# Kernel optimization log

Hardware: AMD Instinct MI355X
Metric: run time of the kernel (lower is better)

Reference implementation:

```python
import jax, jax.numpy as jnp
import numpy as np

B, S, D, H, DK = 32, 1024, 256, 8, 32
MASK_VALUE = -1e-30  # note: NOT -inf; masked scores become ~0 pre-softmax, faithful to source


def setup_inputs() -> dict:
    key = jax.random.key(0)
    ks = jax.random.split(key, 7)
    query = jax.random.normal(ks[0], (B, S, D), dtype=jnp.float32)
    key_t = jax.random.normal(ks[1], (B, S, D), dtype=jnp.float32)
    value = jax.random.normal(ks[2], (B, S, D), dtype=jnp.float32)
    # binary observation mask over key positions
    mask = (jax.random.uniform(ks[3], (B, S)) > 0.5).astype(jnp.float32)
    glorot = jax.nn.initializers.glorot_uniform(in_axis=1, out_axis=2)
    Wq = glorot(ks[4], (H, D, DK), jnp.float32)
    Wk = glorot(ks[5], (H, D, DK), jnp.float32)
    Wv = glorot(ks[6], (H, D, DK), jnp.float32)
    return {"query": query, "key": key_t, "value": value, "mask": mask,
            "Wq": Wq, "Wk": Wk, "Wv": Wv}


def reference(query, key, value, mask, Wq, Wk, Wv):
    # per-head projections, vectorized over heads: [B,S,D] x [H,D,DK] -> [B,H,S,DK]
    q = jnp.einsum('bsd,hdk->bhsk', query, Wq)
    k = jnp.einsum('bsd,hdk->bhsk', key, Wk)
    v = jnp.einsum('bsd,hdk->bhsk', value, Wv)
    # raw scores (no 1/sqrt(dk) scaling in source): [B,H,Sq,Sk]
    A = jnp.einsum('bhqk,bhsk->bhqs', q, k)
    m = mask[:, None, None, :]  # [B,1,1,Sk]
    A = m * A + (1.0 - m) * MASK_VALUE  # multiplicative mask, NOT additive
    A = jax.nn.softmax(A, axis=-1)
    out = jnp.einsum('bhqs,bhsk->bhqk', A, v)  # [B,H,Sq,DK]
    # concat heads along last dim, matching torch.cat order
    return out.transpose(0, 2, 1, 3).reshape(B, S, H * DK)
```

## Files before the change

### kernel.cpp

```cpp
#include <hip/hip_runtime.h>
#include <math.h>

#define B_  32
#define S_  1024
#define D_  256
#define H_  8
#define DK_ 32
#define MASKV (-1e-30f)
#define LOG2E 1.44269504f

typedef __attribute__((ext_vector_type(4))) short bf4_t;
typedef __attribute__((ext_vector_type(8))) short bf8_t;
typedef __attribute__((ext_vector_type(4))) float f4_t;

__device__ __forceinline__ unsigned fbits(float x) {
    union { float f; unsigned u; } v; v.f = x; return v.u;
}
__device__ __forceinline__ float bitsf(unsigned u) {
    union { unsigned u; float f; } v; v.u = u; return v.f;
}

#if __has_builtin(__builtin_amdgcn_exp2f)
#define EXP2F(x) __builtin_amdgcn_exp2f(x)
#else
#define EXP2F(x) __expf((x) * 0.69314718f)
#endif

__device__ __forceinline__ void gld16(const void* g, void* l) {
    __builtin_amdgcn_global_load_lds(
        (const __attribute__((address_space(1))) void*)g,
        (__attribute__((address_space(3))) void*)l, 16, 0, 0);
}

#define PSEL 0x07060302u


__global__ __launch_bounds__(256) void prep_w(
    const float* __restrict__ Wq, const float* __restrict__ Wk,
    const float* __restrict__ Wv, short* __restrict__ WpH, short* __restrict__ WpL)
{
    const int a = blockIdx.x >> 3;
    const int h = blockIdx.x & 7;
    const float* W = (a == 0 ? Wq : (a == 1 ? Wk : Wv)) + (size_t)h * 256 * 32;
    const int t = threadIdx.x;
    const int k    = t & 31;
    const int dgrp = t >> 5;
    const int ng   = h * 2 + (k >> 4);
    const int l15  = k & 15;
#pragma unroll
    for (int jj = blockIdx.y * 2; jj < blockIdx.y * 2 + 2; ++jj) {
        const int d0 = jj * 32 + dgrp * 4;
        float x[4];
#pragma unroll
        for (int r = 0; r < 4; ++r) x[r] = W[(size_t)(d0 + r) * 32 + k];
        unsigned hu[4], lu[4];
#pragma unroll
        for (int r = 0; r < 4; ++r) {
            unsigned hb = (fbits(x[r]) + 0x8000u) & 0xFFFF0000u;
            hu[r] = hb;
            lu[r] = fbits(x[r] - bitsf(hb)) + 0x8000u;
        }
        uint2 hp = make_uint2(__builtin_amdgcn_perm(hu[1], hu[0], PSEL),
                              __builtin_amdgcn_perm(hu[3], hu[2], PSEL));
        uint2 lp = make_uint2(__builtin_amdgcn_perm(lu[1], lu[0], PSEL),
                              __builtin_amdgcn_perm(lu[3], lu[2], PSEL));
        const int quad = (d0 >> 3) & 3;
        const int jb   = d0 & 7;
        size_t off = (size_t)a * 65536
                   + ((size_t)(jj * 16 + ng) * 64 + quad * 16 + l15) * 8 + jb;
        *(uint2*)&WpH[off] = hp;
        *(uint2*)&WpL[off] = lp;
    }
}

__global__ __launch_bounds__(256) void proj_kernel(
    const float* __restrict__ Xq, const float* __restrict__ Xk,
    const float* __restrict__ Xv, const float* __restrict__ mask,
    const short* __restrict__ WpH, const short* __restrict__ WpL,
    short* __restrict__ qpH, short* __restrict__ qpL,
    short* __restrict__ kpH, short* __restrict__ kpL,
    short* __restrict__ vpT)
{
    __shared__ __align__(16) short XsH[8192];
    __shared__ __align__(16) short XsL[8192];

    const int a  = blockIdx.y;
    const float* X = (a == 0 ? Xq : (a == 1 ? Xk : Xv));
    const short* WH = WpH + (size_t)a * 65536;
    const short* WL = WpL + (size_t)a * 65536;
    const int m0 = blockIdx.x * 64;

    const int tid  = threadIdx.x;
    const int lane = tid & 63;
    const int wv   = tid >> 6;
    const int l15  = lane & 15;
    const int quad = lane >> 4;

    f4_t acc[4][4];
#pragma unroll
    for (int i = 0; i < 4; ++i)
#pragma unroll
        for (int j = 0; j < 4; ++j) acc[i][j] = (f4_t){0.f, 0.f, 0.f, 0.f};

    const int r    = tid >> 2;
    const int dseg = tid & 3;
    const int tix  = r >> 4;
    const int rl15 = r & 15;

    for (int h2 = 0; h2 < 2; ++h2) {
        __syncthreads();
        {
            const float* xp = X + (size_t)(m0 + r) * 256 + h2 * 128 + dseg * 32;
#pragma unroll
            for (int q = 0; q < 4; ++q) {
                float4 x0 = *(const float4*)(xp + q * 8);
                float4 x1 = *(const float4*)(xp + q * 8 + 4);
                float xv[8] = {x0.x, x0.y, x0.z, x0.w, x1.x, x1.y, x1.z, x1.w};
                bf8_t hi, lo;
#pragma unroll
                for (int j = 0; j < 8; ++j) {
                    unsigned hu = (fbits(xv[j]) + 0x8000u) & 0xFFFF0000u;
                    hi[j] = (short)(hu >> 16);
                    lo[j] = (short)((fbits(xv[j] - bitsf(hu)) + 0x8000u) >> 16);
                }
                const int off = ((dseg * 4 + tix) * 64 + q * 16 + rl15) * 8;
                *(bf8_t*)&XsH[off] = hi;
                *(bf8_t*)&XsL[off] = lo;
            }
        }
        __syncthreads();

#pragma unroll
        for (int kcl = 0; kcl < 4; ++kcl) {
            const int kc = h2 * 4 + kcl;
            bf8_t xH[4], xL[4];
#pragma unroll
            for (int t = 0; t < 4; ++t) {
                xH[t] = *(const bf8_t*)&XsH[((kcl * 4 + t) * 64 + lane) * 8];
                xL[t] = *(const bf8_t*)&XsL[((kcl * 4 + t) * 64 + lane) * 8];
            }
#pragma unroll
            for (int ns = 0; ns < 4; ++ns) {
                const size_t wo = ((size_t)(kc * 16 + wv * 4 + ns) * 64 + lane) * 8;
                bf8_t wh = *(const bf8_t*)&WH[wo];
                bf8_t wl = *(const bf8_t*)&WL[wo];
#pragma unroll
                for (int t = 0; t < 4; ++t) {
                    f4_t c = acc[t][ns];
                    if (a < 2) {
                        c = __builtin_amdgcn_mfma_f32_16x16x32_bf16(wh, xH[t], c, 0, 0, 0);
                        c = __builtin_amdgcn_mfma_f32_16x16x32_bf16(wl, xH[t], c, 0, 0, 0);
                        c = __builtin_amdgcn_mfma_f32_16x16x32_bf16(wh, xL[t], c, 0, 0, 0);
                    } else {
                        c = __builtin_amdgcn_mfma_f32_16x16x32_bf16(xH[t], wh, c, 0, 0, 0);
                        c = __builtin_amdgcn_mfma_f32_16x16x32_bf16(xH[t], wl, c, 0, 0, 0);
                        c = __builtin_amdgcn_mfma_f32_16x16x32_bf16(xL[t], wh, c, 0, 0, 0);
                    }
                    acc[t][ns] = c;
                }
            }
        }
    }

    const int b  = m0 >> 10;
    const int sB = m0 & 1023;
    if (a < 2) {
        short* dH = (a == 0) ? qpH : kpH;
        short* dL = (a == 0) ? qpL : kpL;
        const float* mbp = mask + (size_t)b * 1024;
#pragma unroll
        for (int t = 0; t < 4; ++t) {
            const int s = sB + t * 16 + l15;
            const float scale = (a == 0) ? LOG2E : mbp[s];
            const int grp = (sB >> 4) + t;
#pragma unroll
            for (int ns = 0; ns < 4; ++ns) {
                const int h_    = wv * 2 + (ns >> 1);
                const int quadA = (ns & 1) * 2 + (quad >> 1);
                const int jb    = (quad & 1) * 4;
                unsigned hu[4], lu[4];
#pragma unroll
                for (int rr = 0; rr < 4; ++rr) {
                    float x = acc[t][ns][rr] * scale;
                    unsigned h32 = fbits(x) + 0x8000u;
                    hu[rr] = h32;
                    float hf = bitsf(h32 & 0xFFFF0000u);
                    lu[rr] = fbits(x - hf) + 0x8000u;
                }
                uint2 hp = make_uint2(__builtin_amdgcn_perm(hu[1], hu[0], PSEL),
                                      __builtin_amdgcn_perm(hu[3], hu[2], PSEL));
                uint2 lp = make_uint2(__builtin_amdgcn_perm(lu[1], lu[0], PSEL),
                                      __builtin_amdgcn_perm(lu[3], lu[2], PSEL));
                size_t off = (((size_t)(b * 8 + h_) * 64 + grp) * 64
                              + quadA * 16 + l15) * 8 + jb;
                *(uint2*)&dH[off] = hp;
                *(uint2*)&dL[off] = lp;
            }
        }
    } else {
#pragma unroll
        for (int t = 0; t < 4; ++t) {
            int sr = sB + t * 16 + quad * 4;
#pragma unroll
            for (int ns = 0; ns < 4; ++ns) {
                int n = wv * 64 + ns * 16 + l15;
                int h = n >> 5, k = n & 31;
                unsigned eu[4];
#pragma unroll
                for (int rr = 0; rr < 4; ++rr) eu[rr] = fbits(acc[t][ns][rr]) + 0x8000u;
                uint2 pk = make_uint2(__builtin_amdgcn_perm(eu[1], eu[0], PSEL),
                                      __builtin_amdgcn_perm(eu[3], eu[2], PSEL));
                *(uint2*)&vpT[((size_t)(b * 8 + h) * 32 + k) * 1024 + sr] = pk;
            }
        }
    }
}

__global__ __launch_bounds__(256) void attn_kernel(
    const short* __restrict__ qpH, const short* __restrict__ qpL,
    const short* __restrict__ kpH, const short* __restrict__ kpL,
    const short* __restrict__ vpT, float* __restrict__ out)
{
    __shared__ __align__(16) short KsH[2][2048];
    __shared__ __align__(16) short KsL[2][2048];
    __shared__ __align__(16) short VsT[2][32 * 72];

    const int tid  = threadIdx.x;
    const int lane = tid & 63;
    const int wv   = tid >> 6;
    const int l15  = lane & 15;
    const int quad = lane >> 4;

    const int L  = (blockIdx.z * gridDim.y + blockIdx.y) * gridDim.x + blockIdx.x;
    const int li = L >> 3;
    const int bh = (L & 7) * 32 + (li >> 3);
    const int qt = li & 7;
    const int b  = bh >> 3;
    const int h  = bh & 7;
    const int woff = qt * 128 + wv * 32;

    bf8_t qh[2], ql[2];
#pragma unroll
    for (int qs = 0; qs < 2; ++qs) {
        const int grp = qt * 8 + wv * 2 + qs;
        size_t off = (((size_t)bh * 64 + grp) * 64 + lane) * 8;
        qh[qs] = *(const bf8_t*)&qpH[off];
        ql[qs] = *(const bf8_t*)&qpL[off];
    }

    f4_t accO[2][2];
    f4_t accS[2];
#pragma unroll
    for (int i = 0; i < 2; ++i) {
        accS[i] = (f4_t){0.f, 0.f, 0.f, 0.f};
#pragma unroll
        for (int j = 0; j < 2; ++j) accO[i][j] = (f4_t){0.f, 0.f, 0.f, 0.f};
    }
    const bf4_t ones4 = {(short)0x3F80, (short)0x3F80, (short)0x3F80, (short)0x3F80};

    const int dv = tid >> 3, seg = tid & 7;

    bf4_t vA[8], vB[8];
    bf4_t pfA[2][4], pfB[2][4];

#define TILE(KT, CUR, DO_STAGE, DO_PV, VIN, VOUT, PIN, POUT)                    \
    {                                                                           \
                      \
        _Pragma("unroll")                                                       \
        for (int ks = 0; ks < 4; ++ks) {                                        \
            VOUT[ks * 2]     = *(const bf4_t*)&VsT[CUR][l15 * 72 + ks * 16 + quad * 4];       \
            VOUT[ks * 2 + 1] = *(const bf4_t*)&VsT[CUR][(16 + l15) * 72 + ks * 16 + quad * 4];\
        }                                                                       \
                    \
        uint4 vreg;                                                             \
        if (DO_STAGE) {                                                         \
            size_t toff = ((size_t)bh * 64 + (size_t)((KT) + 1) * 4) * 512;     \
            gld16(kpH + toff + wv * 512 + lane * 8, (char*)KsH[(CUR) ^ 1] + wv * 1024); \
            gld16(kpL + toff + wv * 512 + lane * 8, (char*)KsL[(CUR) ^ 1] + wv * 1024); \
            vreg = *(const uint4*)&vpT[((size_t)bh * 32 + dv) * 1024            \
                                       + (size_t)((KT) + 1) * 64 + seg * 8];    \
        }                                                                       \
        __builtin_amdgcn_s_setprio(1);                                          \
                       \
        _Pragma("unroll")                                                       \
        for (int ks = 0; ks < 4; ++ks) {                                        \
            bf8_t kh = *(const bf8_t*)&KsH[CUR][ks * 512 + lane * 8];           \
            bf8_t kl = *(const bf8_t*)&KsL[CUR][ks * 512 + lane * 8];           \
            f4_t sc[2];                                                         \
            _Pragma("unroll")                                                   \
            for (int qs = 0; qs < 2; ++qs) {                                    \
                f4_t c = __builtin_amdgcn_mfma_f32_16x16x32_bf16(kh, qh[qs],    \
                             (f4_t){0.f, 0.f, 0.f, 0.f}, 0, 0, 0);              \
                c = __builtin_amdgcn_mfma_f32_16x16x32_bf16(kl, qh[qs], c, 0, 0, 0); \
                c = __builtin_amdgcn_mfma_f32_16x16x32_bf16(kh, ql[qs], c, 0, 0, 0); \
                sc[qs] = c;                                                     \
            }                                                                   \
            if (DO_PV) {                                                        \
                _Pragma("unroll")                                               \
                for (int qs = 0; qs < 2; ++qs) {                                \
                    accO[qs][0] = __builtin_amdgcn_mfma_f32_16x16x16bf16_1k(    \
                                      VIN[ks * 2], PIN[qs][ks], accO[qs][0], 0, 0, 0);     \
                    accO[qs][1] = __builtin_amdgcn_mfma_f32_16x16x16bf16_1k(    \
                                      VIN[ks * 2 + 1], PIN[qs][ks], accO[qs][1], 0, 0, 0); \
                    accS[qs]    = __builtin_amdgcn_mfma_f32_16x16x16bf16_1k(    \
                                      ones4, PIN[qs][ks], accS[qs], 0, 0, 0);   \
                }                                                               \
            }                                                                   \
            _Pragma("unroll")                                                   \
            for (int qs = 0; qs < 2; ++qs) {                                    \
                unsigned eu[4];                                                 \
                _Pragma("unroll")                                               \
                for (int r = 0; r < 4; ++r)                                     \
                    eu[r] = fbits(EXP2F(sc[qs][r])) + 0x8000u;                  \
                union { uint2 u; bf4_t v; } cv;                                 \
                cv.u = make_uint2(__builtin_amdgcn_perm(eu[1], eu[0], PSEL),    \
                                  __builtin_amdgcn_perm(eu[3], eu[2], PSEL));   \
                POUT[qs][ks] = cv.v;                                            \
            }                                                                   \
        }                                                                       \
        __builtin_amdgcn_s_setprio(0);                                          \
                 \
        if (DO_STAGE) *(uint4*)&VsT[(CUR) ^ 1][dv * 72 + seg * 8] = vreg;       \
        __syncthreads();                                                        \
    }

    {
        size_t toff = ((size_t)bh * 64) * 512;
        gld16(kpH + toff + wv * 512 + lane * 8, (char*)KsH[0] + wv * 1024);
        gld16(kpL + toff + wv * 512 + lane * 8, (char*)KsL[0] + wv * 1024);
        uint4 v0 = *(const uint4*)&vpT[((size_t)bh * 32 + dv) * 1024 + seg * 8];
        *(uint4*)&VsT[0][dv * 72 + seg * 8] = v0;
    }
    __syncthreads();

    TILE(0, 0, 1, 0, vA, vA, pfA, pfA)
    for (int i = 0; i < 7; ++i) {
        TILE(2 * i + 1, 1, 1, 1, vA, vB, pfA, pfB)
        TILE(2 * i + 2, 0, 1, 1, vB, vA, pfB, pfA)
    }
    TILE(15, 1, 0, 1, vA, vB, pfA, pfB)

#pragma unroll
    for (int ks = 0; ks < 4; ++ks) {
#pragma unroll
        for (int qs = 0; qs < 2; ++qs) {
            accO[qs][0] = __builtin_amdgcn_mfma_f32_16x16x16bf16_1k(
                              vB[ks * 2], pfB[qs][ks], accO[qs][0], 0, 0, 0);
            accO[qs][1] = __builtin_amdgcn_mfma_f32_16x16x16bf16_1k(
                              vB[ks * 2 + 1], pfB[qs][ks], accO[qs][1], 0, 0, 0);
            accS[qs]    = __builtin_amdgcn_mfma_f32_16x16x16bf16_1k(
                              ones4, pfB[qs][ks], accS[qs], 0, 0, 0);
        }
    }
#undef TILE

#pragma unroll
    for (int qs = 0; qs < 2; ++qs) {
        float inv = 1.0f / accS[qs][0];
        int s = woff + qs * 16 + l15;
        float* op = out + ((size_t)b * 1024 + s) * 256 + h * 32;
#pragma unroll
        for (int dvs = 0; dvs < 2; ++dvs) {
            float4 o4 = make_float4(accO[qs][dvs][0] * inv, accO[qs][dvs][1] * inv,
                                    accO[qs][dvs][2] * inv, accO[qs][dvs][3] * inv);
            *(float4*)&op[dvs * 16 + quad * 4] = o4;
        }
    }
}

extern "C" void kernel_launch(void* const* d_in, const int* in_sizes, int n_in,
                              void* d_out, int out_size, void* d_ws, size_t ws_size,
                              hipStream_t stream)
{
    const float* query = (const float*)d_in[0];
    const float* key   = (const float*)d_in[1];
    const float* value = (const float*)d_in[2];
    const float* mask  = (const float*)d_in[3];
    const float* Wq    = (const float*)d_in[4];
    const float* Wk    = (const float*)d_in[5];
    const float* Wv    = (const float*)d_in[6];
    float* out = (float*)d_out;

    const size_t per = (size_t)B_ * H_ * S_ * DK_;
    short* qpH = (short*)d_ws;
    short* qpL = qpH + per;
    short* kpH = qpL + per;
    short* kpL = kpH + per;
    short* vpT = kpL + per;
    short* WpH = vpT + per;
    short* WpL = WpH + 3 * 256 * 256;

    prep_w<<<dim3(24, 4), 256, 0, stream>>>(Wq, Wk, Wv, WpH, WpL);
    proj_kernel<<<dim3(512, 3), 256, 0, stream>>>(query, key, value, mask, WpH, WpL,
                                                  qpH, qpL, kpH, kpL, vpT);
    attn_kernel<<<dim3(8, H_, B_), 256, 0, stream>>>(qpH, qpL, kpH, kpL, vpT, out);
}
```

Baseline: 271.9 us.

## Double-buffer weight fragments in projection GEMM and drop rounding in P packing

The projection loop is unrolled so the weight hi/lo fragments for the next k-chunk are loaded into a second register buffer while MFMAs run on the current one. This aims to hide global-load latency behind the matrix math. It costs extra VGPRs, which may lower occupancy. Separately, the softmax exponent is now truncated to bf16 instead of rounded, saving one add per element at a small accuracy cost.

```diff
diff --git a/kernel.cpp b/kernel.cpp
--- a/kernel.cpp
+++ b/kernel.cpp
@@ -107,60 +107,87 @@
     const int tix  = r >> 4;
     const int rl15 = r & 15;
 
-    for (int h2 = 0; h2 < 2; ++h2) {
-        __syncthreads();
-        {
-            const float* xp = X + (size_t)(m0 + r) * 256 + h2 * 128 + dseg * 32;
-#pragma unroll
-            for (int q = 0; q < 4; ++q) {
-                float4 x0 = *(const float4*)(xp + q * 8);
-                float4 x1 = *(const float4*)(xp + q * 8 + 4);
-                float xv[8] = {x0.x, x0.y, x0.z, x0.w, x1.x, x1.y, x1.z, x1.w};
-                bf8_t hi, lo;
-#pragma unroll
-                for (int j = 0; j < 8; ++j) {
-                    unsigned hu = (fbits(xv[j]) + 0x8000u) & 0xFFFF0000u;
-                    hi[j] = (short)(hu >> 16);
-                    lo[j] = (short)((fbits(xv[j] - bitsf(hu)) + 0x8000u) >> 16);
-                }
-                const int off = ((dseg * 4 + tix) * 64 + q * 16 + rl15) * 8;
-                *(bf8_t*)&XsH[off] = hi;
-                *(bf8_t*)&XsL[off] = lo;
-            }
-        }
-        __syncthreads();
-
-#pragma unroll
-        for (int kcl = 0; kcl < 4; ++kcl) {
-            const int kc = h2 * 4 + kcl;
-            bf8_t xH[4], xL[4];
-#pragma unroll
-            for (int t = 0; t < 4; ++t) {
-                xH[t] = *(const bf8_t*)&XsH[((kcl * 4 + t) * 64 + lane) * 8];
-                xL[t] = *(const bf8_t*)&XsL[((kcl * 4 + t) * 64 + lane) * 8];
-            }
-#pragma unroll
-            for (int ns = 0; ns < 4; ++ns) {
-                const size_t wo = ((size_t)(kc * 16 + wv * 4 + ns) * 64 + lane) * 8;
-                bf8_t wh = *(const bf8_t*)&WH[wo];
-                bf8_t wl = *(const bf8_t*)&WL[wo];
-#pragma unroll
-                for (int t = 0; t < 4; ++t) {
-                    f4_t c = acc[t][ns];
-                    if (a < 2) {
-                        c = __builtin_amdgcn_mfma_f32_16x16x32_bf16(wh, xH[t], c, 0, 0, 0);
-                        c = __builtin_amdgcn_mfma_f32_16x16x32_bf16(wl, xH[t], c, 0, 0, 0);
-                        c = __builtin_amdgcn_mfma_f32_16x16x32_bf16(wh, xL[t], c, 0, 0, 0);
-                    } else {
-                        c = __builtin_amdgcn_mfma_f32_16x16x32_bf16(xH[t], wh, c, 0, 0, 0);
-                        c = __builtin_amdgcn_mfma_f32_16x16x32_bf16(xH[t], wl, c, 0, 0, 0);
-                        c = __builtin_amdgcn_mfma_f32_16x16x32_bf16(xL[t], wh, c, 0, 0, 0);
-                    }
-                    acc[t][ns] = c;
-                }
-            }
-        }
-    }
+    const short* WHb = WH + (wv * 4) * 512 + lane * 8;
+    const short* WLb = WL + (wv * 4) * 512 + lane * 8;
+
+    bf8_t wAh[4], wAl[4], wBh[4], wBl[4];
+
+#define WLOAD(BUFh, BUFl, KC)                                                  \
+    _Pragma("unroll")                                                          \
+    for (int ns = 0; ns < 4; ++ns) {                                           \
+        BUFh[ns] = *(const bf8_t*)&WHb[(KC) * 8192 + ns * 512];                \
+        BUFl[ns] = *(const bf8_t*)&WLb[(KC) * 8192 + ns * 512];                \
+    }
+
+#define STAGE_X(H2)                                                            \
+    {                                                                          \
+        const float* xp = X + (size_t)(m0 + r) * 256 + (H2) * 128 + dseg * 32; \
+        _Pragma("unroll")                                                      \
+        for (int q = 0; q < 4; ++q) {                                          \
+            float4 x0 = *(const float4*)(xp + q * 8);                          \
+            float4 x1 = *(const float4*)(xp + q * 8 + 4);                      \
+            float xv[8] = {x0.x, x0.y, x0.z, x0.w, x1.x, x1.y, x1.z, x1.w};    \
+            bf8_t hi, lo;                                                      \
+            _Pragma("unroll")                                                  \
+            for (int j = 0; j < 8; ++j) {                                      \
+                unsigned hu = (fbits(xv[j]) + 0x8000u) & 0xFFFF0000u;          \
+                hi[j] = (short)(hu >> 16);                                     \
+                lo[j] = (short)((fbits(xv[j] - bitsf(hu)) + 0x8000u) >> 16);   \
+            }                                                                  \
+            const int off = ((dseg * 4 + tix) * 64 + q * 16 + rl15) * 8;       \
+            *(bf8_t*)&XsH[off] = hi;                                           \
+            *(bf8_t*)&XsL[off] = lo;                                           \
+        }                                                                      \
+    }
+
+#define COMPUTE(KCL, BUFh, BUFl)                                               \
+    {                                                                          \
+        bf8_t xH[4], xL[4];                                                    \
+        _Pragma("unroll")                                                      \
+        for (int t = 0; t < 4; ++t) {                                          \
+            xH[t] = *(const bf8_t*)&XsH[(((KCL) * 4 + t) * 64 + lane) * 8];    \
+            xL[t] = *(const bf8_t*)&XsL[(((KCL) * 4 + t) * 64 + lane) * 8];    \
+        }                                                                      \
+        _Pragma("unroll")                                                      \
+        for (int ns = 0; ns < 4; ++ns) {                                       \
+            _Pragma("unroll")                                                  \
+            for (int t = 0; t < 4; ++t) {                                      \
+                f4_t c = acc[t][ns];                                           \
+                if (a < 2) {                                                   \
+                    c = __builtin_amdgcn_mfma_f32_16x16x32_bf16(BUFh[ns], xH[t], c, 0, 0, 0); \
+                    c = __builtin_amdgcn_mfma_f32_16x16x32_bf16(BUFl[ns], xH[t], c, 0, 0, 0); \
+                    c = __builtin_amdgcn_mfma_f32_16x16x32_bf16(BUFh[ns], xL[t], c, 0, 0, 0); \
+                } else {                                                       \
+                    c = __builtin_amdgcn_mfma_f32_16x16x32_bf16(xH[t], BUFh[ns], c, 0, 0, 0); \
+                    c = __builtin_amdgcn_mfma_f32_16x16x32_bf16(xH[t], BUFl[ns], c, 0, 0, 0); \
+                    c = __builtin_amdgcn_mfma_f32_16x16x32_bf16(xL[t], BUFh[ns], c, 0, 0, 0); \
+                }                                                              \
+                acc[t][ns] = c;                                                \
+            }                                                                  \
+        }                                                                      \
+    }
+
+    WLOAD(wAh, wAl, 0)
+    STAGE_X(0)
+    __syncthreads();
+
+    WLOAD(wBh, wBl, 1)  COMPUTE(0, wAh, wAl)
+    WLOAD(wAh, wAl, 2)  COMPUTE(1, wBh, wBl)
+    WLOAD(wBh, wBl, 3)  COMPUTE(2, wAh, wAl)
+    WLOAD(wAh, wAl, 4)  COMPUTE(3, wBh, wBl)
+
+    __syncthreads();
+    STAGE_X(1)
+    __syncthreads();
+
+    WLOAD(wBh, wBl, 5)  COMPUTE(0, wAh, wAl)
+    WLOAD(wAh, wAl, 6)  COMPUTE(1, wBh, wBl)
+    WLOAD(wBh, wBl, 7)  COMPUTE(2, wAh, wAl)
+                        COMPUTE(3, wBh, wBl)
+
+#undef WLOAD
+#undef STAGE_X
+#undef COMPUTE
 
     const int b  = m0 >> 10;
     const int sB = m0 & 1023;
@@ -311,7 +338,7 @@
                 unsigned eu[4];                                                 \
                 _Pragma("unroll")                                               \
                 for (int r = 0; r < 4; ++r)                                     \
-                    eu[r] = fbits(EXP2F(sc[qs][r])) + 0x8000u;                  \
+                    eu[r] = fbits(EXP2F(sc[qs][r]));      \
                 union { uint2 u; bf4_t v; } cv;                                 \
                 cv.u = make_uint2(__builtin_amdgcn_perm(eu[1], eu[0], PSEL),    \
                                   __builtin_amdgcn_perm(eu[3], eu[2], PSEL));   \
```

Result: faster. 265.2 us (-2.5%).
